# Optimization experiments

Measured on AMD Instinct MI355X. Metric: run time of the kernel, lower is better.

The kernel has to match this reference:

```python
import jax, jax.numpy as jnp
import numpy as np

B, L, F, H, DIM = 32, 1024, 1024, 1024, 1024


def setup_inputs() -> dict:
    key = jax.random.key(0)
    ks = jax.random.split(key, 8)
    features = jax.random.normal(ks[0], (B, L, F), dtype=jnp.float32)
    hidden = jax.random.normal(ks[1], (B, H), dtype=jnp.float32)
    # Dense layer params (glorot-ish scale)
    W1 = jax.random.normal(ks[2], (F, DIM), dtype=jnp.float32) / np.sqrt(F)
    b1 = jnp.zeros((DIM,), dtype=jnp.float32)
    W2 = jax.random.normal(ks[3], (H, DIM), dtype=jnp.float32) / np.sqrt(H)
    b2 = jnp.zeros((DIM,), dtype=jnp.float32)
    Wp = jax.random.normal(ks[4], (DIM, 1), dtype=jnp.float32) / np.sqrt(DIM)
    bp = jnp.zeros((1,), dtype=jnp.float32)
    return {"features": features, "hidden": hidden, "W1": W1, "b1": b1,
            "W2": W2, "b2": b2, "Wp": Wp, "bp": bp}


def reference(features, hidden, W1, b1, W2, b2, Wp, bp):
    # features: [B, L, F], hidden: [B, H]
    h1 = jnp.einsum('blf,fd->bld', features, W1) + b1          # [B, L, D]
    h2 = (hidden @ W2 + b2)[:, None, :]                         # [B, 1, D]
    att = jnp.tanh(h1 + h2)                                     # [B, L, D]
    score = jnp.einsum('bld,do->blo', att, Wp) + bp             # [B, L, 1]
    attention_weights = jax.nn.softmax(score, axis=1)           # [B, L, 1]
    context_vector = jnp.sum(attention_weights * features, axis=1)  # [B, F]
    return context_vector
```

## Files before the change

### kernel.cpp

```cpp
#include <hip/hip_runtime.h>
#include <hip/hip_bf16.h>


typedef __attribute__((ext_vector_type(8))) __bf16 bf16x8;
typedef __attribute__((ext_vector_type(4))) float f32x4;

#define BM 128
#define BN 128
#define LDK 40

static __device__ __forceinline__ ushort f2bf(float x) {
  unsigned u = __float_as_uint(x);
  return (ushort)((u + 0x7fffu + ((u >> 16) & 1u)) >> 16);
}

typedef __attribute__((address_space(1))) void gbl_t;
typedef __attribute__((address_space(3))) void lds_t;
static __device__ __forceinline__ void gl_lds16(const void* g, void* l) {
  __builtin_amdgcn_global_load_lds((gbl_t*)g, (lds_t*)l, 16, 0, 0);
}

static __device__ __forceinline__ bf16x8 cvt8(float4 lo, float4 hi) {
  __hip_bfloat162 c0 = __float22bfloat162_rn({lo.x, lo.y});
  __hip_bfloat162 c1 = __float22bfloat162_rn({lo.z, lo.w});
  __hip_bfloat162 c2 = __float22bfloat162_rn({hi.x, hi.y});
  __hip_bfloat162 c3 = __float22bfloat162_rn({hi.z, hi.w});
  union { int4 i; bf16x8 v; } u;
  u.i.x = *(int*)&c0; u.i.y = *(int*)&c1; u.i.z = *(int*)&c2; u.i.w = *(int*)&c3;
  return u.v;
}

static __device__ __forceinline__ float tanh_fast(float x) {
  float e = __expf(2.f * x);
  return 1.f - 2.f / (e + 1.f);
}

__global__ __launch_bounds__(256) void prep_kernel(
    const float* __restrict__ feat_half, ushort* __restrict__ featb,
    const float* __restrict__ W1, ushort* __restrict__ w1t,
    const float* __restrict__ hidden, const float* __restrict__ W2,
    const float* __restrict__ b2, float* __restrict__ h2p, int cvt_blocks) {
  __shared__ float smem[64 * 65];
  const int bx = blockIdx.x, tid = threadIdx.x;
  if (bx < cvt_blocks) {
    const size_t i8 = ((size_t)bx * 256 + tid) * 8;
    float4 a = *(const float4*)(feat_half + i8);
    float4 c = *(const float4*)(feat_half + i8 + 4);
    union { bf16x8 v; int4 i; } u;
    u.v = cvt8(a, c);
    *(int4*)(featb + i8) = u.i;
  } else if (bx < cvt_blocks + 256) {
    const int t = bx - cvt_blocks;
    const int tc = t & 15, tr = t >> 4;
    float (*tt)[65] = (float(*)[65])smem;
    const int r = tid >> 4, c4 = (tid & 15) * 4;
#pragma unroll
    for (int p = 0; p < 4; ++p) {
      const int rr = p * 16 + r;
      float4 v = *(const float4*)(W1 + (size_t)(tr * 64 + rr) * 1024 + tc * 64 + c4);
      tt[rr][c4] = v.x; tt[rr][c4 + 1] = v.y; tt[rr][c4 + 2] = v.z; tt[rr][c4 + 3] = v.w;
    }
    __syncthreads();
    const int cc = tid >> 3, r8 = (tid & 7) * 8;
#pragma unroll
    for (int p = 0; p < 2; ++p) {
      const int c = p * 32 + cc;
      ushort tmp[8];
#pragma unroll
      for (int j = 0; j < 8; ++j) tmp[j] = f2bf(tt[r8 + j][c]);
      *(int4*)(w1t + (size_t)(tc * 64 + c) * 1024 + tr * 64 + r8) = *(int4*)tmp;
    }
  } else {
    const int t = bx - cvt_blocks - 256;
    const int dblk = t & 3, b = (t >> 2) & 31, z = t >> 7;
    const int d = dblk * 256 + tid;
    const int k0 = z * 128;
    float* h = smem;
    if (tid < 128) h[tid] = hidden[b * 1024 + k0 + tid];
    __syncthreads();
    float acc = (z == 0) ? b2[d] : 0.f;
#pragma unroll 8
    for (int k = 0; k < 128; ++k)
      acc += h[k] * W2[(size_t)(k0 + k) * 1024 + d];
    h2p[z * 32768 + b * 1024 + d] = acc;
  }
}

#define GEMM_PRELOOP()                                                         \
  if (tid < 128) {                                                             \
    const int d = col0 + tid;                                                  \
    float hv = b1[d];                                                          \
    _Pragma("unroll") for (int p = 0; p < 8; ++p)                              \
        hv += h2p[p * 32768 + b * 1024 + d];                                   \
    hbl[tid] = hv;                                                             \
  } else {                                                                     \
    wpl[tid - 128] = wp[col0 + tid - 128];                                     \
  }

#define GEMM_EPILOGUE(ROWG)                                                    \
  float hbv[4], wpv[4];                                                        \
  _Pragma("unroll") for (int j = 0; j < 4; ++j) {                              \
    const int idx = wn * 64 + j * 16 + lrow;                                   \
    hbv[j] = hbl[idx];                                                         \
    wpv[j] = wpl[idx];                                                         \
  }                                                                            \
  float rsum[4][4];                                                            \
  _Pragma("unroll") for (int i = 0; i < 4; ++i) {                              \
    _Pragma("unroll") for (int r = 0; r < 4; ++r) {                            \
      float s = 0.f;                                                           \
      _Pragma("unroll") for (int j = 0; j < 4; ++j)                            \
          s += tanh_fast(acc[i][j][r] + hbv[j]) * wpv[j];                      \
      s += __shfl_xor(s, 8);                                                   \
      s += __shfl_xor(s, 4);                                                   \
      s += __shfl_xor(s, 2);                                                   \
      s += __shfl_xor(s, 1);                                                   \
      rsum[i][r] = s;                                                          \
    }                                                                          \
  }                                                                            \
  if (wn == 1 && lrow == 0) {                                                  \
    _Pragma("unroll") for (int i = 0; i < 4; ++i)                              \
        _Pragma("unroll") for (int r = 0; r < 4; ++r)                          \
            sred[wm][i * 16 + quad * 4 + r] = rsum[i][r];                      \
  }                                                                            \
  __syncthreads();                                                             \
  if (wn == 0 && lrow == 0) {                                                  \
    _Pragma("unroll") for (int i = 0; i < 4; ++i)                              \
        _Pragma("unroll") for (int r = 0; r < 4; ++r) {                        \
          const int ro = wm * 64 + i * 16 + quad * 4 + r;                      \
          score_p[(size_t)blockIdx.y * 32768 + (ROWG) + ro] =                  \
              rsum[i][r] + sred[wm][ro & 63];                                  \
        }                                                                      \
  }

__global__ __launch_bounds__(256) void gemm_score_bf16_kernel(
    const ushort* __restrict__ featb,
    const ushort* __restrict__ w1t,
    const float* __restrict__ b1, const float* __restrict__ h2p,
    const float* __restrict__ wp, float* __restrict__ score_p,
    int row_base) {
  __shared__ ushort ldsA[BM * 64];
  __shared__ ushort ldsB[BN * 64];
  __shared__ float sred[2][64];
  __shared__ float hbl[128], wpl[128];
  const int tid = threadIdx.x;
  const int row0 = blockIdx.x * BM;
  const int col0 = blockIdx.y * BN;
  const int b = (row_base + row0) >> 10;

  const int wave = tid >> 6, lane = tid & 63;
  const int wm = wave & 1, wn = wave >> 1;
  const int lrow = lane & 15, quad = lane >> 4;

  GEMM_PRELOOP()

  int a_go[4], b_go[4], ls[4];
#pragma unroll
  for (int it = 0; it < 4; ++it) {
    const int slot = wave * 256 + it * 64 + lane;
    const int r = slot >> 3, c = slot & 7;
    const int gc = c ^ (r & 7);
    a_go[it] = (row0 + r) * 1024 + gc * 8;
    b_go[it] = (col0 + r) * 1024 + gc * 8;
    ls[it] = (wave * 256 + it * 64) * 16;
  }

  f32x4 acc[4][4] = {};

  for (int k0 = 0; k0 < 1024; k0 += 64) {
#pragma unroll
    for (int it = 0; it < 4; ++it)
      gl_lds16(featb + a_go[it] + k0, (char*)ldsA + ls[it]);
#pragma unroll
    for (int it = 0; it < 4; ++it)
      gl_lds16(w1t + b_go[it] + k0, (char*)ldsB + ls[it]);
    __syncthreads();

#pragma unroll
    for (int s = 0; s < 2; ++s) {
      bf16x8 af[4], bfr[4];
#pragma unroll
      for (int i = 0; i < 4; ++i) {
        const int r = wm * 64 + i * 16 + lrow;
        af[i] = *(const bf16x8*)&ldsA[r * 64 + (((s * 4 + quad) ^ (r & 7)) * 8)];
      }
#pragma unroll
      for (int j = 0; j < 4; ++j) {
        const int r = wn * 64 + j * 16 + lrow;
        bfr[j] = *(const bf16x8*)&ldsB[r * 64 + (((s * 4 + quad) ^ (r & 7)) * 8)];
      }
#pragma unroll
      for (int i = 0; i < 4; ++i)
#pragma unroll
        for (int j = 0; j < 4; ++j)
          acc[i][j] = __builtin_amdgcn_mfma_f32_16x16x32_bf16(
              af[i], bfr[j], acc[i][j], 0, 0, 0);
    }
    __syncthreads();
  }

  GEMM_EPILOGUE(row_base + row0)
}

__global__ __launch_bounds__(256) void gemm_score_cvt_kernel(
    const float* __restrict__ feat, const ushort* __restrict__ w1t,
    const float* __restrict__ b1, const float* __restrict__ h2p,
    const float* __restrict__ wp, float* __restrict__ score_p) {
  __shared__ ushort ldsA[BM * LDK];
  __shared__ ushort ldsB[BN * LDK];
  __shared__ float sred[2][64];
  __shared__ float hbl[128], wpl[128];
  const int tid = threadIdx.x;
  const int row0 = blockIdx.x * BM;
  const int col0 = blockIdx.y * BN;
  const int b = row0 >> 10;

  const int wave = tid >> 6, lane = tid & 63;
  const int wm = wave & 1, wn = wave >> 1;
  const int lrow = lane & 15, quad = lane >> 4;

  GEMM_PRELOOP()

  const int arow = tid >> 1;
  const int akof = (tid & 1) * 16;
  const int brow = tid >> 2;
  const int bkof = (tid & 3) * 8;

  f32x4 acc[4][4] = {};

  for (int k0 = 0; k0 < 1024; k0 += 32) {
    {
      const float* ap = feat + (size_t)(row0 + arow) * 1024 + k0 + akof;
      float4 v0 = *(const float4*)(ap + 0);
      float4 v1 = *(const float4*)(ap + 4);
      float4 v2 = *(const float4*)(ap + 8);
      float4 v3 = *(const float4*)(ap + 12);
      union { bf16x8 v; int4 i; } w0, w1;
      w0.v = cvt8(v0, v1);
      w1.v = cvt8(v2, v3);
      *(int4*)&ldsA[arow * LDK + akof] = w0.i;
      *(int4*)&ldsA[arow * LDK + akof + 8] = w1.i;
    }
#pragma unroll
    for (int p = 0; p < 2; ++p) {
      const int m = p * 64 + brow;
      *(int4*)&ldsB[m * LDK + bkof] =
          *(const int4*)(w1t + (size_t)(col0 + m) * 1024 + k0 + bkof);
    }
    __syncthreads();
    bf16x8 af[4], bfr[4];
#pragma unroll
    for (int i = 0; i < 4; ++i)
      af[i] = *(const bf16x8*)&ldsA[(wm * 64 + i * 16 + lrow) * LDK + quad * 8];
#pragma unroll
    for (int j = 0; j < 4; ++j)
      bfr[j] = *(const bf16x8*)&ldsB[(wn * 64 + j * 16 + lrow) * LDK + quad * 8];
#pragma unroll
    for (int i = 0; i < 4; ++i)
#pragma unroll
      for (int j = 0; j < 4; ++j)
        acc[i][j] = __builtin_amdgcn_mfma_f32_16x16x32_bf16(
            af[i], bfr[j], acc[i][j], 0, 0, 0);
    __syncthreads();
  }

  GEMM_EPILOGUE(row0)
}

__global__ __launch_bounds__(256) void softmax_kernel(
    const float* __restrict__ score_p, float* __restrict__ w,
    float* __restrict__ out) {
  const int b = blockIdx.x, tid = threadIdx.x;
  const int lane = tid & 63, wv = tid >> 6;
  __shared__ float sm[4], ss[4];
  float v[4];
  float mx = -1e30f;
#pragma unroll
  for (int i = 0; i < 4; ++i) {
    const int idx = b * 1024 + i * 256 + tid;
    out[idx] = 0.f;
    float s = 0.f;
#pragma unroll
    for (int p = 0; p < 8; ++p) s += score_p[p * 32768 + idx];
    v[i] = s;
    mx = fmaxf(mx, s);
  }
#pragma unroll
  for (int off = 32; off; off >>= 1) mx = fmaxf(mx, __shfl_xor(mx, off));
  if (lane == 0) sm[wv] = mx;
  __syncthreads();
  mx = fmaxf(fmaxf(sm[0], sm[1]), fmaxf(sm[2], sm[3]));
  float sum = 0.f;
#pragma unroll
  for (int i = 0; i < 4; ++i) {
    v[i] = __expf(v[i] - mx);
    sum += v[i];
  }
#pragma unroll
  for (int off = 32; off; off >>= 1) sum += __shfl_xor(sum, off);
  if (lane == 0) ss[wv] = sum;
  __syncthreads();
  const float inv = 1.f / (ss[0] + ss[1] + ss[2] + ss[3]);
#pragma unroll
  for (int i = 0; i < 4; ++i) w[b * 1024 + i * 256 + tid] = v[i] * inv;
}

__global__ __launch_bounds__(256) void context_kernel(
    const float* __restrict__ w, const float* __restrict__ feat,
    float* __restrict__ out) {
  const int b = blockIdx.y;
  const int l0 = blockIdx.x * 64;
  const int f0 = threadIdx.x * 4;
  __shared__ float wl[64];
  if (threadIdx.x < 64) wl[threadIdx.x] = w[b * 1024 + l0 + threadIdx.x];
  __syncthreads();
  const float* fb = feat + (size_t)b * 1048576 + (size_t)l0 * 1024 + f0;
  float a0 = 0.f, a1 = 0.f, a2 = 0.f, a3 = 0.f;
#pragma unroll 8
  for (int l = 0; l < 64; ++l) {
    float4 v = *(const float4*)(fb + (size_t)l * 1024);
    const float wv = wl[l];
    a0 += wv * v.x;
    a1 += wv * v.y;
    a2 += wv * v.z;
    a3 += wv * v.w;
  }
  float* dst = out + b * 1024 + f0;
  atomicAdd(dst + 0, a0);
  atomicAdd(dst + 1, a1);
  atomicAdd(dst + 2, a2);
  atomicAdd(dst + 3, a3);
}

extern "C" void kernel_launch(void* const* d_in, const int* in_sizes, int n_in,
                              void* d_out, int out_size, void* d_ws, size_t ws_size,
                              hipStream_t stream) {
  const float* feat   = (const float*)d_in[0];
  const float* hidden = (const float*)d_in[1];
  const float* W1     = (const float*)d_in[2];
  const float* b1     = (const float*)d_in[3];
  const float* W2     = (const float*)d_in[4];
  const float* b2     = (const float*)d_in[5];
  const float* Wp     = (const float*)d_in[6];
  float* out = (float*)d_out;

  char* ws = (char*)d_ws;
  ushort* w1t    = (ushort*)ws;
  float* score_p = (float*)(ws + 2097152);
  float* h2p     = (float*)(ws + 3145728);
  float* wts     = (float*)(ws + 4194304);
  ushort* featb  = (ushort*)(ws + 4325376);
  const bool big_ws = ws_size >= (size_t)(4325376 + 33554432);

  if (big_ws) {
    prep_kernel<<<9472, 256, 0, stream>>>(feat, featb, W1, w1t, hidden, W2, b2,
                                          h2p, 8192);
    gemm_score_bf16_kernel<<<dim3(128, 8), 256, 0, stream>>>(
        featb, w1t, b1, h2p, Wp, score_p, 0);
    prep_kernel<<<8192, 256, 0, stream>>>(feat + 16777216, featb, W1, w1t,
                                          hidden, W2, b2, h2p, 8192);
    gemm_score_bf16_kernel<<<dim3(128, 8), 256, 0, stream>>>(
        featb, w1t, b1, h2p, Wp, score_p, 16384);
  } else {
    prep_kernel<<<1280, 256, 0, stream>>>(feat, featb, W1, w1t, hidden, W2, b2,
                                          h2p, 0);
    gemm_score_cvt_kernel<<<dim3(256, 8), 256, 0, stream>>>(feat, w1t, b1, h2p,
                                                            Wp, score_p);
  }

  softmax_kernel<<<32, 256, 0, stream>>>(score_p, wts, out);
  context_kernel<<<dim3(16, 32), 256, 0, stream>>>(wts, feat, out);
}
```

Before: 339.3 us.

## Use 256x256 eight-phase pipelined bf16 GEMM with single full-batch conversion pass

After: 328.6 us. 1.03x faster.

```diff
diff --git a/kernel.cpp b/kernel.cpp
--- a/kernel.cpp
+++ b/kernel.cpp
@@ -8,6 +8,7 @@
 #define BM 128
 #define BN 128
 #define LDK 40
+#define NT 16
 
 static __device__ __forceinline__ ushort f2bf(float x) {
   unsigned u = __float_as_uint(x);
@@ -83,6 +84,179 @@
     for (int k = 0; k < 128; ++k)
       acc += h[k] * W2[(size_t)(k0 + k) * 1024 + d];
     h2p[z * 32768 + b * 1024 + d] = acc;
+  }
+}
+
+
+#define PH_BAR1() { asm volatile("" ::: "memory"); __builtin_amdgcn_s_barrier(); }
+#define PH_BAR2() { __builtin_amdgcn_sched_barrier(0); asm volatile("" ::: "memory"); __builtin_amdgcn_s_barrier(); }
+
+#define STAGE_A(TILE, KH, BUF) {                                               \
+    const int ko_ = (TILE) * 64 + (KH) * 32;                                   \
+    gl_lds16(featb + a_off[0] + ko_, (char*)&ldsA[BUF][KH][0][0] + l_off0);    \
+    gl_lds16(featb + a_off[1] + ko_, (char*)&ldsA[BUF][KH][0][0] + l_off1); }
+#define STAGE_B(TILE, KH, BUF) {                                               \
+    const int ko_ = (TILE) * 64 + (KH) * 32;                                   \
+    gl_lds16(w1t + b_off[0] + ko_, (char*)&ldsB[BUF][KH][0][0] + l_off0);      \
+    gl_lds16(w1t + b_off[1] + ko_, (char*)&ldsB[BUF][KH][0][0] + l_off1); }
+
+#define LDA_F(I, S, BUF, DST) {                                                \
+    const int r_ = wm * 128 + (I) * 16 + lrow;                                 \
+    DST = *(const bf16x8*)&ldsA[BUF][S][r_][(quad ^ ((r_ >> 1) & 3)) * 8]; }
+#define LDB_F(J, S, BUF, DST) {                                                \
+    const int r_ = wn * 64 + (J) * 16 + lrow;                                  \
+    DST = *(const bf16x8*)&ldsB[BUF][S][r_][(quad ^ ((r_ >> 1) & 3)) * 8]; }
+
+#define MFMA4(IB, AF)                                                          \
+  acc[IB][0] = __builtin_amdgcn_mfma_f32_16x16x32_bf16(AF, bf0, acc[IB][0], 0, 0, 0); \
+  acc[IB][1] = __builtin_amdgcn_mfma_f32_16x16x32_bf16(AF, bf1, acc[IB][1], 0, 0, 0); \
+  acc[IB][2] = __builtin_amdgcn_mfma_f32_16x16x32_bf16(AF, bf2, acc[IB][2], 0, 0, 0); \
+  acc[IB][3] = __builtin_amdgcn_mfma_f32_16x16x32_bf16(AF, bf3, acc[IB][3], 0, 0, 0);
+
+__global__ __launch_bounds__(512, 2) void gemm_score_8ph_kernel(
+    const ushort* __restrict__ featb,
+    const ushort* __restrict__ w1t,
+    const float* __restrict__ b1, const float* __restrict__ h2p,
+    const float* __restrict__ wp, float* __restrict__ score_p) {
+  __shared__ ushort ldsA[2][2][256][32];
+  __shared__ ushort ldsB[2][2][256][32];
+  __shared__ float hbl[256], wpl[256];
+  __shared__ float sred[2][3][128];
+
+  const int tid = threadIdx.x;
+  const int row0 = blockIdx.x * 256;
+  const int col0 = blockIdx.y * 256;
+  const int b = row0 >> 10;
+  const int wave = tid >> 6, lane = tid & 63;
+  const int wm = wave >> 2, wn = wave & 3;
+  const int lrow = lane & 15, quad = lane >> 4;
+
+  if (tid < 256) {
+    const int d = col0 + tid;
+    float hv = b1[d];
+#pragma unroll
+    for (int p = 0; p < 8; ++p) hv += h2p[p * 32768 + b * 1024 + d];
+    hbl[tid] = hv;
+  } else {
+    wpl[tid - 256] = wp[col0 + tid - 256];
+  }
+
+  int a_off[2], b_off[2];
+  int l_off0, l_off1;
+  {
+    const int s0 = wave * 128 + lane;
+    const int r0 = s0 >> 2, c0 = s0 & 3;
+    const int q0 = c0 ^ ((r0 >> 1) & 3);
+    a_off[0] = (row0 + r0) * 1024 + q0 * 8;
+    b_off[0] = (col0 + r0) * 1024 + q0 * 8;
+    const int s1 = s0 + 64;
+    const int r1 = s1 >> 2, c1 = s1 & 3;
+    const int q1 = c1 ^ ((r1 >> 1) & 3);
+    a_off[1] = (row0 + r1) * 1024 + q1 * 8;
+    b_off[1] = (col0 + r1) * 1024 + q1 * 8;
+    l_off0 = (wave * 128) * 16;
+    l_off1 = (wave * 128 + 64) * 16;
+  }
+
+  f32x4 acc[8][4] = {};
+
+  STAGE_B(0, 0, 0); STAGE_A(0, 0, 0); STAGE_B(0, 1, 0); STAGE_A(0, 1, 0);
+  asm volatile("s_waitcnt vmcnt(4)" ::: "memory");
+  STAGE_B(1, 0, 1); STAGE_A(1, 0, 1); STAGE_B(1, 1, 1);
+  asm volatile("s_waitcnt vmcnt(6) lgkmcnt(0)" ::: "memory");
+  __builtin_amdgcn_s_barrier();
+
+#pragma unroll 2
+  for (int t = 0; t < NT; ++t) {
+    const int cur = t & 1, nxt = cur ^ 1;
+    bf16x8 af0, af1, af2, af3, bf0, bf1, bf2, bf3;
+
+    LDB_F(0, 0, cur, bf0); LDB_F(1, 0, cur, bf1);
+    LDB_F(2, 0, cur, bf2); LDB_F(3, 0, cur, bf3);
+    LDA_F(0, 0, cur, af0); LDA_F(1, 0, cur, af1);
+    LDA_F(2, 0, cur, af2); LDA_F(3, 0, cur, af3);
+    if (t + 1 < NT) STAGE_A(t + 1, 1, nxt);
+    PH_BAR1();
+    __builtin_amdgcn_s_setprio(1);
+    MFMA4(0, af0); MFMA4(1, af1); MFMA4(2, af2); MFMA4(3, af3);
+    __builtin_amdgcn_s_setprio(0);
+    PH_BAR2();
+
+    LDA_F(4, 0, cur, af0); LDA_F(5, 0, cur, af1);
+    LDA_F(6, 0, cur, af2); LDA_F(7, 0, cur, af3);
+    if (t + 2 < NT) STAGE_B(t + 2, 0, cur);
+    PH_BAR1();
+    __builtin_amdgcn_s_setprio(1);
+    MFMA4(4, af0); MFMA4(5, af1); MFMA4(6, af2); MFMA4(7, af3);
+    __builtin_amdgcn_s_setprio(0);
+    PH_BAR2();
+
+    LDB_F(0, 1, cur, bf0); LDB_F(1, 1, cur, bf1);
+    LDB_F(2, 1, cur, bf2); LDB_F(3, 1, cur, bf3);
+    LDA_F(0, 1, cur, af0); LDA_F(1, 1, cur, af1);
+    LDA_F(2, 1, cur, af2); LDA_F(3, 1, cur, af3);
+    if (t + 2 < NT) STAGE_A(t + 2, 0, cur);
+    PH_BAR1();
+    __builtin_amdgcn_s_setprio(1);
+    MFMA4(0, af0); MFMA4(1, af1); MFMA4(2, af2); MFMA4(3, af3);
+    __builtin_amdgcn_s_setprio(0);
+    PH_BAR2();
+
+    LDA_F(4, 1, cur, af0); LDA_F(5, 1, cur, af1);
+    LDA_F(6, 1, cur, af2); LDA_F(7, 1, cur, af3);
+    if (t + 2 < NT) STAGE_B(t + 2, 1, cur);
+    if (t < NT - 2) {
+      asm volatile("s_waitcnt vmcnt(6)" ::: "memory");
+    } else {
+      asm volatile("s_waitcnt vmcnt(0)" ::: "memory");
+    }
+    PH_BAR1();
+    __builtin_amdgcn_s_setprio(1);
+    MFMA4(4, af0); MFMA4(5, af1); MFMA4(6, af2); MFMA4(7, af3);
+    __builtin_amdgcn_s_setprio(0);
+    PH_BAR2();
+  }
+
+  float hbv[4], wpv[4];
+#pragma unroll
+  for (int j = 0; j < 4; ++j) {
+    const int idx = wn * 64 + j * 16 + lrow;
+    hbv[j] = hbl[idx];
+    wpv[j] = wpl[idx];
+  }
+  float rs[8][4];
+#pragma unroll
+  for (int i = 0; i < 8; ++i) {
+#pragma unroll
+    for (int r = 0; r < 4; ++r) {
+      float s = 0.f;
+#pragma unroll
+      for (int j = 0; j < 4; ++j)
+        s += tanh_fast(acc[i][j][r] + hbv[j]) * wpv[j];
+      s += __shfl_xor(s, 8);
+      s += __shfl_xor(s, 4);
+      s += __shfl_xor(s, 2);
+      s += __shfl_xor(s, 1);
+      rs[i][r] = s;
+    }
+  }
+  if (wn != 0 && lrow == 0) {
+#pragma unroll
+    for (int i = 0; i < 8; ++i)
+#pragma unroll
+      for (int r = 0; r < 4; ++r)
+        sred[wm][wn - 1][i * 16 + quad * 4 + r] = rs[i][r];
+  }
+  __syncthreads();
+  if (wn == 0 && lrow == 0) {
+#pragma unroll
+    for (int i = 0; i < 8; ++i)
+#pragma unroll
+      for (int r = 0; r < 4; ++r) {
+        const int ro = i * 16 + quad * 4 + r;
+        score_p[(size_t)blockIdx.y * 32768 + row0 + wm * 128 + ro] =
+            rs[i][r] + sred[wm][0][ro] + sred[wm][1][ro] + sred[wm][2][ro];
+      }
   }
 }
 
@@ -132,75 +306,6 @@
         }                                                                      \
   }
 
-__global__ __launch_bounds__(256) void gemm_score_bf16_kernel(
-    const ushort* __restrict__ featb,
-    const ushort* __restrict__ w1t,
-    const float* __restrict__ b1, const float* __restrict__ h2p,
-    const float* __restrict__ wp, float* __restrict__ score_p,
-    int row_base) {
-  __shared__ ushort ldsA[BM * 64];
-  __shared__ ushort ldsB[BN * 64];
-  __shared__ float sred[2][64];
-  __shared__ float hbl[128], wpl[128];
-  const int tid = threadIdx.x;
-  const int row0 = blockIdx.x * BM;
-  const int col0 = blockIdx.y * BN;
-  const int b = (row_base + row0) >> 10;
-
-  const int wave = tid >> 6, lane = tid & 63;
-  const int wm = wave & 1, wn = wave >> 1;
-  const int lrow = lane & 15, quad = lane >> 4;
-
-  GEMM_PRELOOP()
-
-  int a_go[4], b_go[4], ls[4];
-#pragma unroll
-  for (int it = 0; it < 4; ++it) {
-    const int slot = wave * 256 + it * 64 + lane;
-    const int r = slot >> 3, c = slot & 7;
-    const int gc = c ^ (r & 7);
-    a_go[it] = (row0 + r) * 1024 + gc * 8;
-    b_go[it] = (col0 + r) * 1024 + gc * 8;
-    ls[it] = (wave * 256 + it * 64) * 16;
-  }
-
-  f32x4 acc[4][4] = {};
-
-  for (int k0 = 0; k0 < 1024; k0 += 64) {
-#pragma unroll
-    for (int it = 0; it < 4; ++it)
-      gl_lds16(featb + a_go[it] + k0, (char*)ldsA + ls[it]);
-#pragma unroll
-    for (int it = 0; it < 4; ++it)
-      gl_lds16(w1t + b_go[it] + k0, (char*)ldsB + ls[it]);
-    __syncthreads();
-
-#pragma unroll
-    for (int s = 0; s < 2; ++s) {
-      bf16x8 af[4], bfr[4];
-#pragma unroll
-      for (int i = 0; i < 4; ++i) {
-        const int r = wm * 64 + i * 16 + lrow;
-        af[i] = *(const bf16x8*)&ldsA[r * 64 + (((s * 4 + quad) ^ (r & 7)) * 8)];
-      }
-#pragma unroll
-      for (int j = 0; j < 4; ++j) {
-        const int r = wn * 64 + j * 16 + lrow;
-        bfr[j] = *(const bf16x8*)&ldsB[r * 64 + (((s * 4 + quad) ^ (r & 7)) * 8)];
-      }
-#pragma unroll
-      for (int i = 0; i < 4; ++i)
-#pragma unroll
-        for (int j = 0; j < 4; ++j)
-          acc[i][j] = __builtin_amdgcn_mfma_f32_16x16x32_bf16(
-              af[i], bfr[j], acc[i][j], 0, 0, 0);
-    }
-    __syncthreads();
-  }
-
-  GEMM_EPILOGUE(row_base + row0)
-}
-
 __global__ __launch_bounds__(256) void gemm_score_cvt_kernel(
     const float* __restrict__ feat, const ushort* __restrict__ w1t,
     const float* __restrict__ b1, const float* __restrict__ h2p,
@@ -268,7 +373,7 @@
 
 __global__ __launch_bounds__(256) void softmax_kernel(
     const float* __restrict__ score_p, float* __restrict__ w,
-    float* __restrict__ out) {
+    float* __restrict__ out, int np) {
   const int b = blockIdx.x, tid = threadIdx.x;
   const int lane = tid & 63, wv = tid >> 6;
   __shared__ float sm[4], ss[4];
@@ -279,8 +384,7 @@
     const int idx = b * 1024 + i * 256 + tid;
     out[idx] = 0.f;
     float s = 0.f;
-#pragma unroll
-    for (int p = 0; p < 8; ++p) s += score_p[p * 32768 + idx];
+    for (int p = 0; p < np; ++p) s += score_p[p * 32768 + idx];
     v[i] = s;
     mx = fmaxf(mx, s);
   }
@@ -349,24 +453,21 @@
   float* h2p     = (float*)(ws + 3145728);
   float* wts     = (float*)(ws + 4194304);
   ushort* featb  = (ushort*)(ws + 4325376);
-  const bool big_ws = ws_size >= (size_t)(4325376 + 33554432);
+  const bool big_ws = ws_size >= (size_t)(4325376 + 67108864);
 
   if (big_ws) {
-    prep_kernel<<<9472, 256, 0, stream>>>(feat, featb, W1, w1t, hidden, W2, b2,
-                                          h2p, 8192);
-    gemm_score_bf16_kernel<<<dim3(128, 8), 256, 0, stream>>>(
-        featb, w1t, b1, h2p, Wp, score_p, 0);
-    prep_kernel<<<8192, 256, 0, stream>>>(feat + 16777216, featb, W1, w1t,
-                                          hidden, W2, b2, h2p, 8192);
-    gemm_score_bf16_kernel<<<dim3(128, 8), 256, 0, stream>>>(
-        featb, w1t, b1, h2p, Wp, score_p, 16384);
+    prep_kernel<<<17664, 256, 0, stream>>>(feat, featb, W1, w1t, hidden, W2, b2,
+                                           h2p, 16384);
+    gemm_score_8ph_kernel<<<dim3(128, 4), 512, 0, stream>>>(featb, w1t, b1, h2p,
+                                                            Wp, score_p);
+    softmax_kernel<<<32, 256, 0, stream>>>(score_p, wts, out, 4);
   } else {
     prep_kernel<<<1280, 256, 0, stream>>>(feat, featb, W1, w1t, hidden, W2, b2,
                                           h2p, 0);
     gemm_score_cvt_kernel<<<dim3(256, 8), 256, 0, stream>>>(feat, w1t, b1, h2p,
                                                             Wp, score_p);
-  }
-
-  softmax_kernel<<<32, 256, 0, stream>>>(score_p, wts, out);
+    softmax_kernel<<<32, 256, 0, stream>>>(score_p, wts, out, 8);
+  }
+
   context_kernel<<<dim3(16, 32), 256, 0, stream>>>(wts, feat, out);
 }
```

## Replace bf16 score GEMM with double-buffered 128x256 tile kernel and single pass

Applied to the files above, without the earlier changes.

New measurement: 332.7 us. No clear change (-1.9%).

```diff
diff --git a/kernel.cpp b/kernel.cpp
--- a/kernel.cpp
+++ b/kernel.cpp
@@ -83,6 +83,126 @@
     for (int k = 0; k < 128; ++k)
       acc += h[k] * W2[(size_t)(k0 + k) * 1024 + d];
     h2p[z * 32768 + b * 1024 + d] = acc;
+  }
+}
+
+
+#define STAGE_A32(T, BUF) {                                                    \
+    gl_lds16(featb + a_go + (T) * 32,         (char*)ldsA + (BUF) * 8192 + lA);\
+    gl_lds16(featb + a_go + 65536 + (T) * 32, (char*)ldsA + (BUF) * 8192 + lA + 4096); }
+#define STAGE_B32(T, BUF) {                                                    \
+    gl_lds16(w1t + b_go + (T) * 32,          (char*)ldsB + (BUF) * 16384 + lA);\
+    gl_lds16(w1t + b_go + 65536 + (T) * 32,  (char*)ldsB + (BUF) * 16384 + lA + 4096); \
+    gl_lds16(w1t + b_go + 131072 + (T) * 32, (char*)ldsB + (BUF) * 16384 + lA + 8192); \
+    gl_lds16(w1t + b_go + 196608 + (T) * 32, (char*)ldsB + (BUF) * 16384 + lA + 12288); }
+
+#define MFMA_B16(AF, IB)                                                       \
+  acc[IB][0] = __builtin_amdgcn_mfma_f32_16x16x32_bf16(AF, bfr0, acc[IB][0], 0, 0, 0); \
+  acc[IB][1] = __builtin_amdgcn_mfma_f32_16x16x32_bf16(AF, bfr1, acc[IB][1], 0, 0, 0); \
+  acc[IB][2] = __builtin_amdgcn_mfma_f32_16x16x32_bf16(AF, bfr2, acc[IB][2], 0, 0, 0); \
+  acc[IB][3] = __builtin_amdgcn_mfma_f32_16x16x32_bf16(AF, bfr3, acc[IB][3], 0, 0, 0);
+
+#define TILE32(T, CUR, NXT) {                                                  \
+    if ((T) + 1 < 32) { STAGE_A32((T) + 1, NXT); STAGE_B32((T) + 1, NXT); }    \
+    bf16x8 bfr0, bfr1, bfr2, bfr3;                                             \
+    bfr0 = *(const bf16x8*)&ldsB[CUR][wave * 64 + lrow][cswz8];                \
+    bfr1 = *(const bf16x8*)&ldsB[CUR][wave * 64 + 16 + lrow][cswz8];           \
+    bfr2 = *(const bf16x8*)&ldsB[CUR][wave * 64 + 32 + lrow][cswz8];           \
+    bfr3 = *(const bf16x8*)&ldsB[CUR][wave * 64 + 48 + lrow][cswz8];           \
+    _Pragma("unroll") for (int i = 0; i < 8; ++i) {                            \
+      const bf16x8 af = *(const bf16x8*)&ldsA[CUR][i * 16 + lrow][cswz8];      \
+      MFMA_B16(af, i)                                                          \
+    }                                                                          \
+    __syncthreads();                                                           \
+  }
+
+__global__ __launch_bounds__(256, 2) void gemm_score_tlp_kernel(
+    const ushort* __restrict__ featb,
+    const ushort* __restrict__ w1t,
+    const float* __restrict__ b1, const float* __restrict__ h2p,
+    const float* __restrict__ wp, float* __restrict__ score_p) {
+  __shared__ ushort ldsA[2][128][32];
+  __shared__ ushort ldsB[2][256][32];
+  __shared__ float hbl[256], wpl[256];
+  __shared__ float sred[3][128];
+
+  const int tid = threadIdx.x;
+  const int row0 = blockIdx.x * 128;
+  const int col0 = blockIdx.y * 256;
+  const int b = blockIdx.x >> 3;
+  const int wave = tid >> 6, lane = tid & 63;
+  const int lrow = lane & 15, quad = lane >> 4;
+  const int cswz8 = (quad ^ ((lrow >> 1) & 3)) * 8;
+
+  {
+    const int d = col0 + tid;
+    float hv = b1[d];
+#pragma unroll
+    for (int p = 0; p < 8; ++p) hv += h2p[p * 32768 + b * 1024 + d];
+    hbl[tid] = hv;
+    wpl[tid] = wp[d];
+  }
+
+  int a_go, b_go, lA;
+  {
+    const int s = wave * 64 + lane;
+    const int r = s >> 2, c = s & 3;
+    const int q = c ^ ((r >> 1) & 3);
+    a_go = (row0 + r) * 1024 + q * 8;
+    b_go = (col0 + r) * 1024 + q * 8;
+    lA = (wave * 64) * 16;
+  }
+
+  f32x4 acc[8][4] = {};
+
+  STAGE_A32(0, 0); STAGE_B32(0, 0);
+  __syncthreads();
+
+  for (int t = 0; t < 32; t += 2) {
+    TILE32(t, 0, 1);
+    TILE32(t + 1, 1, 0);
+  }
+
+  float hbv[4], wpv[4];
+#pragma unroll
+  for (int j = 0; j < 4; ++j) {
+    const int idx = wave * 64 + j * 16 + lrow;
+    hbv[j] = hbl[idx];
+    wpv[j] = wpl[idx];
+  }
+  float rs[8][4];
+#pragma unroll
+  for (int i = 0; i < 8; ++i) {
+#pragma unroll
+    for (int r = 0; r < 4; ++r) {
+      float s = 0.f;
+#pragma unroll
+      for (int j = 0; j < 4; ++j)
+        s += tanh_fast(acc[i][j][r] + hbv[j]) * wpv[j];
+      s += __shfl_xor(s, 8);
+      s += __shfl_xor(s, 4);
+      s += __shfl_xor(s, 2);
+      s += __shfl_xor(s, 1);
+      rs[i][r] = s;
+    }
+  }
+  if (wave != 0 && lrow == 0) {
+#pragma unroll
+    for (int i = 0; i < 8; ++i)
+#pragma unroll
+      for (int r = 0; r < 4; ++r)
+        sred[wave - 1][i * 16 + quad * 4 + r] = rs[i][r];
+  }
+  __syncthreads();
+  if (wave == 0 && lrow == 0) {
+#pragma unroll
+    for (int i = 0; i < 8; ++i)
+#pragma unroll
+      for (int r = 0; r < 4; ++r) {
+        const int ro = i * 16 + quad * 4 + r;
+        score_p[(size_t)blockIdx.y * 32768 + row0 + ro] =
+            rs[i][r] + sred[0][ro] + sred[1][ro] + sred[2][ro];
+      }
   }
 }
 
@@ -132,75 +252,6 @@
         }                                                                      \
   }
 
-__global__ __launch_bounds__(256) void gemm_score_bf16_kernel(
-    const ushort* __restrict__ featb,
-    const ushort* __restrict__ w1t,
-    const float* __restrict__ b1, const float* __restrict__ h2p,
-    const float* __restrict__ wp, float* __restrict__ score_p,
-    int row_base) {
-  __shared__ ushort ldsA[BM * 64];
-  __shared__ ushort ldsB[BN * 64];
-  __shared__ float sred[2][64];
-  __shared__ float hbl[128], wpl[128];
-  const int tid = threadIdx.x;
-  const int row0 = blockIdx.x * BM;
-  const int col0 = blockIdx.y * BN;
-  const int b = (row_base + row0) >> 10;
-
-  const int wave = tid >> 6, lane = tid & 63;
-  const int wm = wave & 1, wn = wave >> 1;
-  const int lrow = lane & 15, quad = lane >> 4;
-
-  GEMM_PRELOOP()
-
-  int a_go[4], b_go[4], ls[4];
-#pragma unroll
-  for (int it = 0; it < 4; ++it) {
-    const int slot = wave * 256 + it * 64 + lane;
-    const int r = slot >> 3, c = slot & 7;
-    const int gc = c ^ (r & 7);
-    a_go[it] = (row0 + r) * 1024 + gc * 8;
-    b_go[it] = (col0 + r) * 1024 + gc * 8;
-    ls[it] = (wave * 256 + it * 64) * 16;
-  }
-
-  f32x4 acc[4][4] = {};
-
-  for (int k0 = 0; k0 < 1024; k0 += 64) {
-#pragma unroll
-    for (int it = 0; it < 4; ++it)
-      gl_lds16(featb + a_go[it] + k0, (char*)ldsA + ls[it]);
-#pragma unroll
-    for (int it = 0; it < 4; ++it)
-      gl_lds16(w1t + b_go[it] + k0, (char*)ldsB + ls[it]);
-    __syncthreads();
-
-#pragma unroll
-    for (int s = 0; s < 2; ++s) {
-      bf16x8 af[4], bfr[4];
-#pragma unroll
-      for (int i = 0; i < 4; ++i) {
-        const int r = wm * 64 + i * 16 + lrow;
-        af[i] = *(const bf16x8*)&ldsA[r * 64 + (((s * 4 + quad) ^ (r & 7)) * 8)];
-      }
-#pragma unroll
-      for (int j = 0; j < 4; ++j) {
-        const int r = wn * 64 + j * 16 + lrow;
-        bfr[j] = *(const bf16x8*)&ldsB[r * 64 + (((s * 4 + quad) ^ (r & 7)) * 8)];
-      }
-#pragma unroll
-      for (int i = 0; i < 4; ++i)
-#pragma unroll
-        for (int j = 0; j < 4; ++j)
-          acc[i][j] = __builtin_amdgcn_mfma_f32_16x16x32_bf16(
-              af[i], bfr[j], acc[i][j], 0, 0, 0);
-    }
-    __syncthreads();
-  }
-
-  GEMM_EPILOGUE(row_base + row0)
-}
-
 __global__ __launch_bounds__(256) void gemm_score_cvt_kernel(
     const float* __restrict__ feat, const ushort* __restrict__ w1t,
     const float* __restrict__ b1, const float* __restrict__ h2p,
@@ -268,7 +319,7 @@
 
 __global__ __launch_bounds__(256) void softmax_kernel(
     const float* __restrict__ score_p, float* __restrict__ w,
-    float* __restrict__ out) {
+    float* __restrict__ out, int np) {
   const int b = blockIdx.x, tid = threadIdx.x;
   const int lane = tid & 63, wv = tid >> 6;
   __shared__ float sm[4], ss[4];
@@ -279,8 +330,7 @@
     const int idx = b * 1024 + i * 256 + tid;
     out[idx] = 0.f;
     float s = 0.f;
-#pragma unroll
-    for (int p = 0; p < 8; ++p) s += score_p[p * 32768 + idx];
+    for (int p = 0; p < np; ++p) s += score_p[p * 32768 + idx];
     v[i] = s;
     mx = fmaxf(mx, s);
   }
@@ -349,24 +399,21 @@
   float* h2p     = (float*)(ws + 3145728);
   float* wts     = (float*)(ws + 4194304);
   ushort* featb  = (ushort*)(ws + 4325376);
-  const bool big_ws = ws_size >= (size_t)(4325376 + 33554432);
+  const bool big_ws = ws_size >= (size_t)(4325376 + 67108864);
 
   if (big_ws) {
-    prep_kernel<<<9472, 256, 0, stream>>>(feat, featb, W1, w1t, hidden, W2, b2,
-                                          h2p, 8192);
-    gemm_score_bf16_kernel<<<dim3(128, 8), 256, 0, stream>>>(
-        featb, w1t, b1, h2p, Wp, score_p, 0);
-    prep_kernel<<<8192, 256, 0, stream>>>(feat + 16777216, featb, W1, w1t,
-                                          hidden, W2, b2, h2p, 8192);
-    gemm_score_bf16_kernel<<<dim3(128, 8), 256, 0, stream>>>(
-        featb, w1t, b1, h2p, Wp, score_p, 16384);
+    prep_kernel<<<17664, 256, 0, stream>>>(feat, featb, W1, w1t, hidden, W2, b2,
+                                           h2p, 16384);
+    gemm_score_tlp_kernel<<<dim3(256, 4), 256, 0, stream>>>(featb, w1t, b1, h2p,
+                                                            Wp, score_p);
+    softmax_kernel<<<32, 256, 0, stream>>>(score_p, wts, out, 4);
   } else {
     prep_kernel<<<1280, 256, 0, stream>>>(feat, featb, W1, w1t, hidden, W2, b2,
                                           h2p, 0);
     gemm_score_cvt_kernel<<<dim3(256, 8), 256, 0, stream>>>(feat, w1t, b1, h2p,
                                                             Wp, score_p);
-  }
-
-  softmax_kernel<<<32, 256, 0, stream>>>(score_p, wts, out);
+    softmax_kernel<<<32, 256, 0, stream>>>(score_p, wts, out, 8);
+  }
+
   context_kernel<<<dim3(16, 32), 256, 0, stream>>>(wts, feat, out);
 }
```

## Fuse fp32-to-bf16 conversion into GEMM with register-prefetched double-buffered A tiles

Applied to the files above, without the earlier changes.

New measurement: 398.0 us. 17.3% more time.

```diff
diff --git a/kernel.cpp b/kernel.cpp
--- a/kernel.cpp
+++ b/kernel.cpp
@@ -4,20 +4,10 @@
 
 typedef __attribute__((ext_vector_type(8))) __bf16 bf16x8;
 typedef __attribute__((ext_vector_type(4))) float f32x4;
-
-#define BM 128
-#define BN 128
-#define LDK 40
 
 static __device__ __forceinline__ ushort f2bf(float x) {
   unsigned u = __float_as_uint(x);
   return (ushort)((u + 0x7fffu + ((u >> 16) & 1u)) >> 16);
-}
-
-typedef __attribute__((address_space(1))) void gbl_t;
-typedef __attribute__((address_space(3))) void lds_t;
-static __device__ __forceinline__ void gl_lds16(const void* g, void* l) {
-  __builtin_amdgcn_global_load_lds((gbl_t*)g, (lds_t*)l, 16, 0, 0);
 }
 
 static __device__ __forceinline__ bf16x8 cvt8(float4 lo, float4 hi) {
@@ -36,22 +26,13 @@
 }
 
 __global__ __launch_bounds__(256) void prep_kernel(
-    const float* __restrict__ feat_half, ushort* __restrict__ featb,
     const float* __restrict__ W1, ushort* __restrict__ w1t,
     const float* __restrict__ hidden, const float* __restrict__ W2,
-    const float* __restrict__ b2, float* __restrict__ h2p, int cvt_blocks) {
+    const float* __restrict__ b2, float* __restrict__ h2p) {
   __shared__ float smem[64 * 65];
   const int bx = blockIdx.x, tid = threadIdx.x;
-  if (bx < cvt_blocks) {
-    const size_t i8 = ((size_t)bx * 256 + tid) * 8;
-    float4 a = *(const float4*)(feat_half + i8);
-    float4 c = *(const float4*)(feat_half + i8 + 4);
-    union { bf16x8 v; int4 i; } u;
-    u.v = cvt8(a, c);
-    *(int4*)(featb + i8) = u.i;
-  } else if (bx < cvt_blocks + 256) {
-    const int t = bx - cvt_blocks;
-    const int tc = t & 15, tr = t >> 4;
+  if (bx < 256) {
+    const int tc = bx & 15, tr = bx >> 4;
     float (*tt)[65] = (float(*)[65])smem;
     const int r = tid >> 4, c4 = (tid & 15) * 4;
 #pragma unroll
@@ -71,7 +52,7 @@
       *(int4*)(w1t + (size_t)(tc * 64 + c) * 1024 + tr * 64 + r8) = *(int4*)tmp;
     }
   } else {
-    const int t = bx - cvt_blocks - 256;
+    const int t = bx - 256;
     const int dblk = t & 3, b = (t >> 2) & 31, z = t >> 7;
     const int d = dblk * 256 + tid;
     const int k0 = z * 128;
@@ -86,184 +67,149 @@
   }
 }
 
-#define GEMM_PRELOOP()                                                         \
-  if (tid < 128) {                                                             \
-    const int d = col0 + tid;                                                  \
-    float hv = b1[d];                                                          \
-    _Pragma("unroll") for (int p = 0; p < 8; ++p)                              \
-        hv += h2p[p * 32768 + b * 1024 + d];                                   \
-    hbl[tid] = hv;                                                             \
-  } else {                                                                     \
-    wpl[tid - 128] = wp[col0 + tid - 128];                                     \
-  }
-
-#define GEMM_EPILOGUE(ROWG)                                                    \
-  float hbv[4], wpv[4];                                                        \
-  _Pragma("unroll") for (int j = 0; j < 4; ++j) {                              \
-    const int idx = wn * 64 + j * 16 + lrow;                                   \
-    hbv[j] = hbl[idx];                                                         \
-    wpv[j] = wpl[idx];                                                         \
-  }                                                                            \
-  float rsum[4][4];                                                            \
-  _Pragma("unroll") for (int i = 0; i < 4; ++i) {                              \
-    _Pragma("unroll") for (int r = 0; r < 4; ++r) {                            \
-      float s = 0.f;                                                           \
-      _Pragma("unroll") for (int j = 0; j < 4; ++j)                            \
-          s += tanh_fast(acc[i][j][r] + hbv[j]) * wpv[j];                      \
-      s += __shfl_xor(s, 8);                                                   \
-      s += __shfl_xor(s, 4);                                                   \
-      s += __shfl_xor(s, 2);                                                   \
-      s += __shfl_xor(s, 1);                                                   \
-      rsum[i][r] = s;                                                          \
+
+#define MFMA_ROW(AF, I)                                                        \
+  acc[I][0] = __builtin_amdgcn_mfma_f32_16x16x32_bf16(AF, bf0, acc[I][0], 0, 0, 0); \
+  acc[I][1] = __builtin_amdgcn_mfma_f32_16x16x32_bf16(AF, bf1, acc[I][1], 0, 0, 0); \
+  acc[I][2] = __builtin_amdgcn_mfma_f32_16x16x32_bf16(AF, bf2, acc[I][2], 0, 0, 0); \
+  acc[I][3] = __builtin_amdgcn_mfma_f32_16x16x32_bf16(AF, bf3, acc[I][3], 0, 0, 0);
+
+#define TILE_STEP(T, CUR, NXT, AVIN, AVOUT) {                                  \
+                                                      \
+    bf16x8 bf0 = *(const bf16x8*)(bb + (T) * 32);                              \
+    bf16x8 bf1 = *(const bf16x8*)(bb + 16384 + (T) * 32);                      \
+    bf16x8 bf2 = *(const bf16x8*)(bb + 32768 + (T) * 32);                      \
+    bf16x8 bf3 = *(const bf16x8*)(bb + 49152 + (T) * 32);                      \
+                                                     \
+    if ((T) + 2 < 32) {                                                        \
+      const float* ap_ = feat + (size_t)(row0 + ar) * 1024 + ((T) + 2) * 32 + akof; \
+      AVOUT[0] = *(const float4*)(ap_);                                        \
+      AVOUT[1] = *(const float4*)(ap_ + 4);                                    \
+      AVOUT[2] = *(const float4*)(ap_ + 8);                                    \
+      AVOUT[3] = *(const float4*)(ap_ + 12);                                   \
     }                                                                          \
-  }                                                                            \
-  if (wn == 1 && lrow == 0) {                                                  \
-    _Pragma("unroll") for (int i = 0; i < 4; ++i)                              \
-        _Pragma("unroll") for (int r = 0; r < 4; ++r)                          \
-            sred[wm][i * 16 + quad * 4 + r] = rsum[i][r];                      \
-  }                                                                            \
-  __syncthreads();                                                             \
-  if (wn == 0 && lrow == 0) {                                                  \
-    _Pragma("unroll") for (int i = 0; i < 4; ++i)                              \
-        _Pragma("unroll") for (int r = 0; r < 4; ++r) {                        \
-          const int ro = wm * 64 + i * 16 + quad * 4 + r;                      \
-          score_p[(size_t)blockIdx.y * 32768 + (ROWG) + ro] =                  \
-              rsum[i][r] + sred[wm][ro & 63];                                  \
-        }                                                                      \
-  }
-
-__global__ __launch_bounds__(256) void gemm_score_bf16_kernel(
-    const ushort* __restrict__ featb,
+                                                    \
+    bf16x8 af0 = *(const bf16x8*)&ldsA[CUR][wm * 64 + lrow][cswz8];            \
+    bf16x8 af1 = *(const bf16x8*)&ldsA[CUR][wm * 64 + 16 + lrow][cswz8];       \
+    bf16x8 af2 = *(const bf16x8*)&ldsA[CUR][wm * 64 + 32 + lrow][cswz8];       \
+    bf16x8 af3 = *(const bf16x8*)&ldsA[CUR][wm * 64 + 48 + lrow][cswz8];       \
+    MFMA_ROW(af0, 0); MFMA_ROW(af1, 1); MFMA_ROW(af2, 2); MFMA_ROW(af3, 3);    \
+                                     \
+    if ((T) + 1 < 32) {                                                        \
+      union { bf16x8 v; int4 i; } w0_, w1_;                                    \
+      w0_.v = cvt8(AVIN[0], AVIN[1]);                                          \
+      w1_.v = cvt8(AVIN[2], AVIN[3]);                                          \
+      *(int4*)&ldsA[NXT][ar][awz0] = w0_.i;                                    \
+      *(int4*)&ldsA[NXT][ar][awz1] = w1_.i;                                    \
+    }                                                                          \
+    __syncthreads();                                                           \
+  }
+
+__global__ __launch_bounds__(256, 3) void gemm_score_kernel(
+    const float* __restrict__ feat,
     const ushort* __restrict__ w1t,
     const float* __restrict__ b1, const float* __restrict__ h2p,
-    const float* __restrict__ wp, float* __restrict__ score_p,
-    int row_base) {
-  __shared__ ushort ldsA[BM * 64];
-  __shared__ ushort ldsB[BN * 64];
+    const float* __restrict__ wp, float* __restrict__ score_p) {
+  __shared__ ushort ldsA[2][128][32];
   __shared__ float sred[2][64];
   __shared__ float hbl[128], wpl[128];
+
   const int tid = threadIdx.x;
-  const int row0 = blockIdx.x * BM;
-  const int col0 = blockIdx.y * BN;
-  const int b = (row_base + row0) >> 10;
+  const int row0 = blockIdx.x * 128;
+  const int col0 = blockIdx.y * 128;
+  const int b = blockIdx.x >> 3;
 
   const int wave = tid >> 6, lane = tid & 63;
   const int wm = wave & 1, wn = wave >> 1;
   const int lrow = lane & 15, quad = lane >> 4;
-
-  GEMM_PRELOOP()
-
-  int a_go[4], b_go[4], ls[4];
-#pragma unroll
-  for (int it = 0; it < 4; ++it) {
-    const int slot = wave * 256 + it * 64 + lane;
-    const int r = slot >> 3, c = slot & 7;
-    const int gc = c ^ (r & 7);
-    a_go[it] = (row0 + r) * 1024 + gc * 8;
-    b_go[it] = (col0 + r) * 1024 + gc * 8;
-    ls[it] = (wave * 256 + it * 64) * 16;
-  }
+  const int cswz8 = (quad ^ ((lrow >> 1) & 3)) * 8;
+
+  if (tid < 128) {
+    const int d = col0 + tid;
+    float hv = b1[d];
+#pragma unroll
+    for (int p = 0; p < 8; ++p) hv += h2p[p * 32768 + b * 1024 + d];
+    hbl[tid] = hv;
+  } else {
+    wpl[tid - 128] = wp[col0 + tid - 128];
+  }
+
+  const int ar = tid >> 1;
+  const int akof = (tid & 1) * 16;
+  const int xr = (ar >> 1) & 3;
+  const int awz0 = ((2 * (tid & 1) + 0) ^ xr) * 8;
+  const int awz1 = ((2 * (tid & 1) + 1) ^ xr) * 8;
+
+  const ushort* bb = w1t + (size_t)(col0 + wn * 64 + lrow) * 1024 + quad * 8;
 
   f32x4 acc[4][4] = {};
-
-  for (int k0 = 0; k0 < 1024; k0 += 64) {
-#pragma unroll
-    for (int it = 0; it < 4; ++it)
-      gl_lds16(featb + a_go[it] + k0, (char*)ldsA + ls[it]);
-#pragma unroll
-    for (int it = 0; it < 4; ++it)
-      gl_lds16(w1t + b_go[it] + k0, (char*)ldsB + ls[it]);
-    __syncthreads();
-
-#pragma unroll
-    for (int s = 0; s < 2; ++s) {
-      bf16x8 af[4], bfr[4];
-#pragma unroll
-      for (int i = 0; i < 4; ++i) {
-        const int r = wm * 64 + i * 16 + lrow;
-        af[i] = *(const bf16x8*)&ldsA[r * 64 + (((s * 4 + quad) ^ (r & 7)) * 8)];
+  float4 avA[4], avB[4];
+
+  {
+    const float* ap_ = feat + (size_t)(row0 + ar) * 1024 + akof;
+    float4 v0 = *(const float4*)(ap_);
+    float4 v1 = *(const float4*)(ap_ + 4);
+    float4 v2 = *(const float4*)(ap_ + 8);
+    float4 v3 = *(const float4*)(ap_ + 12);
+    union { bf16x8 v; int4 i; } w0_, w1_;
+    w0_.v = cvt8(v0, v1);
+    w1_.v = cvt8(v2, v3);
+    *(int4*)&ldsA[0][ar][awz0] = w0_.i;
+    *(int4*)&ldsA[0][ar][awz1] = w1_.i;
+    const float* ap1_ = ap_ + 32;
+    avA[0] = *(const float4*)(ap1_);
+    avA[1] = *(const float4*)(ap1_ + 4);
+    avA[2] = *(const float4*)(ap1_ + 8);
+    avA[3] = *(const float4*)(ap1_ + 12);
+  }
+  __syncthreads();
+
+  for (int t = 0; t < 32; t += 2) {
+    TILE_STEP(t, 0, 1, avA, avB);
+    TILE_STEP(t + 1, 1, 0, avB, avA);
+  }
+
+  float hbv[4], wpv[4];
+#pragma unroll
+  for (int j = 0; j < 4; ++j) {
+    const int idx = wn * 64 + j * 16 + lrow;
+    hbv[j] = hbl[idx];
+    wpv[j] = wpl[idx];
+  }
+  float rsum[4][4];
+#pragma unroll
+  for (int i = 0; i < 4; ++i) {
+#pragma unroll
+    for (int r = 0; r < 4; ++r) {
+      float s = 0.f;
+#pragma unroll
+      for (int j = 0; j < 4; ++j)
+        s += tanh_fast(acc[i][j][r] + hbv[j]) * wpv[j];
+      s += __shfl_xor(s, 8);
+      s += __shfl_xor(s, 4);
+      s += __shfl_xor(s, 2);
+      s += __shfl_xor(s, 1);
+      rsum[i][r] = s;
+    }
+  }
+  if (wn == 1 && lrow == 0) {
+#pragma unroll
+    for (int i = 0; i < 4; ++i)
+#pragma unroll
+      for (int r = 0; r < 4; ++r)
+        sred[wm][i * 16 + quad * 4 + r] = rsum[i][r];
+  }
+  __syncthreads();
+  if (wn == 0 && lrow == 0) {
+#pragma unroll
+    for (int i = 0; i < 4; ++i)
+#pragma unroll
+      for (int r = 0; r < 4; ++r) {
+        const int ro = wm * 64 + i * 16 + quad * 4 + r;
+        score_p[(size_t)blockIdx.y * 32768 + row0 + ro] =
+            rsum[i][r] + sred[wm][ro & 63];
       }
-#pragma unroll
-      for (int j = 0; j < 4; ++j) {
-        const int r = wn * 64 + j * 16 + lrow;
-        bfr[j] = *(const bf16x8*)&ldsB[r * 64 + (((s * 4 + quad) ^ (r & 7)) * 8)];
-      }
-#pragma unroll
-      for (int i = 0; i < 4; ++i)
-#pragma unroll
-        for (int j = 0; j < 4; ++j)
-          acc[i][j] = __builtin_amdgcn_mfma_f32_16x16x32_bf16(
-              af[i], bfr[j], acc[i][j], 0, 0, 0);
-    }
-    __syncthreads();
-  }
-
-  GEMM_EPILOGUE(row_base + row0)
-}
-
-__global__ __launch_bounds__(256) void gemm_score_cvt_kernel(
-    const float* __restrict__ feat, const ushort* __restrict__ w1t,
-    const float* __restrict__ b1, const float* __restrict__ h2p,
-    const float* __restrict__ wp, float* __restrict__ score_p) {
-  __shared__ ushort ldsA[BM * LDK];
-  __shared__ ushort ldsB[BN * LDK];
-  __shared__ float sred[2][64];
-  __shared__ float hbl[128], wpl[128];
-  const int tid = threadIdx.x;
-  const int row0 = blockIdx.x * BM;
-  const int col0 = blockIdx.y * BN;
-  const int b = row0 >> 10;
-
-  const int wave = tid >> 6, lane = tid & 63;
-  const int wm = wave & 1, wn = wave >> 1;
-  const int lrow = lane & 15, quad = lane >> 4;
-
-  GEMM_PRELOOP()
-
-  const int arow = tid >> 1;
-  const int akof = (tid & 1) * 16;
-  const int brow = tid >> 2;
-  const int bkof = (tid & 3) * 8;
-
-  f32x4 acc[4][4] = {};
-
-  for (int k0 = 0; k0 < 1024; k0 += 32) {
-    {
-      const float* ap = feat + (size_t)(row0 + arow) * 1024 + k0 + akof;
-      float4 v0 = *(const float4*)(ap + 0);
-      float4 v1 = *(const float4*)(ap + 4);
-      float4 v2 = *(const float4*)(ap + 8);
-      float4 v3 = *(const float4*)(ap + 12);
-      union { bf16x8 v; int4 i; } w0, w1;
-      w0.v = cvt8(v0, v1);
-      w1.v = cvt8(v2, v3);
-      *(int4*)&ldsA[arow * LDK + akof] = w0.i;
-      *(int4*)&ldsA[arow * LDK + akof + 8] = w1.i;
-    }
-#pragma unroll
-    for (int p = 0; p < 2; ++p) {
-      const int m = p * 64 + brow;
-      *(int4*)&ldsB[m * LDK + bkof] =
-          *(const int4*)(w1t + (size_t)(col0 + m) * 1024 + k0 + bkof);
-    }
-    __syncthreads();
-    bf16x8 af[4], bfr[4];
-#pragma unroll
-    for (int i = 0; i < 4; ++i)
-      af[i] = *(const bf16x8*)&ldsA[(wm * 64 + i * 16 + lrow) * LDK + quad * 8];
-#pragma unroll
-    for (int j = 0; j < 4; ++j)
-      bfr[j] = *(const bf16x8*)&ldsB[(wn * 64 + j * 16 + lrow) * LDK + quad * 8];
-#pragma unroll
-    for (int i = 0; i < 4; ++i)
-#pragma unroll
-      for (int j = 0; j < 4; ++j)
-        acc[i][j] = __builtin_amdgcn_mfma_f32_16x16x32_bf16(
-            af[i], bfr[j], acc[i][j], 0, 0, 0);
-    __syncthreads();
-  }
-
-  GEMM_EPILOGUE(row0)
+  }
 }
 
 __global__ __launch_bounds__(256) void softmax_kernel(
@@ -348,25 +294,10 @@
   float* score_p = (float*)(ws + 2097152);
   float* h2p     = (float*)(ws + 3145728);
   float* wts     = (float*)(ws + 4194304);
-  ushort* featb  = (ushort*)(ws + 4325376);
-  const bool big_ws = ws_size >= (size_t)(4325376 + 33554432);
-
-  if (big_ws) {
-    prep_kernel<<<9472, 256, 0, stream>>>(feat, featb, W1, w1t, hidden, W2, b2,
-                                          h2p, 8192);
-    gemm_score_bf16_kernel<<<dim3(128, 8), 256, 0, stream>>>(
-        featb, w1t, b1, h2p, Wp, score_p, 0);
-    prep_kernel<<<8192, 256, 0, stream>>>(feat + 16777216, featb, W1, w1t,
-                                          hidden, W2, b2, h2p, 8192);
-    gemm_score_bf16_kernel<<<dim3(128, 8), 256, 0, stream>>>(
-        featb, w1t, b1, h2p, Wp, score_p, 16384);
-  } else {
-    prep_kernel<<<1280, 256, 0, stream>>>(feat, featb, W1, w1t, hidden, W2, b2,
-                                          h2p, 0);
-    gemm_score_cvt_kernel<<<dim3(256, 8), 256, 0, stream>>>(feat, w1t, b1, h2p,
-                                                            Wp, score_p);
-  }
-
+
+  prep_kernel<<<1280, 256, 0, stream>>>(W1, w1t, hidden, W2, b2, h2p);
+  gemm_score_kernel<<<dim3(256, 8), 256, 0, stream>>>(feat, w1t, b1, h2p, Wp,
+                                                      score_p);
   softmax_kernel<<<32, 256, 0, stream>>>(score_p, wts, out);
   context_kernel<<<dim3(16, 32), 256, 0, stream>>>(wts, feat, out);
 }
```
